# Kernel optimization log

Hardware: AMD Instinct MI355X
Metric: run time of the kernel (lower is better)

The kernel has to match this reference:

```python
import jax, jax.numpy as jnp
import numpy as np

B, S, D = 2, 1024, 1024
N_HEADS = 16
R = 128
M = 8
N_NEURONS = 256


def group_gate(gate, n_basis):
    # gate: [B,S,N] -> [B,S,M], sum over consecutive groups, then normalize
    b, s, n = gate.shape
    gs = n // n_basis  # exact by construction (256/8)
    g = gate.reshape(b, s, n_basis, gs).sum(axis=-1)
    return g / (g.sum(axis=-1, keepdims=True) + 1e-8)


def feature_fn(x, neurons, weights):
    # x:[B,S,D], neurons:[M,D,R], weights:[B,S,M] -> h:[B,S,R]
    all_h = jnp.einsum('bsd,mdr->bsmr', x, neurons)
    return jnp.einsum('bsmr,bsm->bsr', all_h, weights)


def restore_fn(h, neurons, weights):
    # h:[B,S,R], neurons:[M,R,D], weights:[B,S,M] -> [B,S,D]
    pre = jnp.einsum('bsr,bsm->bsmr', h, weights)
    return jnp.einsum('bsmr,mrd->bsd', pre, neurons)


def setup_inputs() -> dict:
    key = jax.random.key(0)
    ks = jax.random.split(key, 9)
    sc = 0.02
    return {
        'x': jax.random.normal(ks[0], (B, S, D), jnp.float32),
        'qk_f': jax.random.normal(ks[1], (M, D, R), jnp.float32) * sc,
        'qk_r': jax.random.normal(ks[2], (M, R, D), jnp.float32) * sc,
        'v_f': jax.random.normal(ks[3], (M, D, R), jnp.float32) * sc,
        'v_r': jax.random.normal(ks[4], (M, R, D), jnp.float32) * sc,
        'Wg_q': jax.random.normal(ks[5], (D, N_NEURONS), jnp.float32) * sc,
        'Wg_k': jax.random.normal(ks[6], (D, N_NEURONS), jnp.float32) * sc,
        'Wg_v': jax.random.normal(ks[7], (D, N_NEURONS), jnp.float32) * sc,
        'W_O': jax.random.normal(ks[8], (D, D), jnp.float32) * sc,
    }


def reference(x, qk_f, qk_r, v_f, v_r, Wg_q, Wg_k, Wg_v, W_O):
    # Router gates (softmax over neuron dim), then grouped per basis
    g_Q = jax.nn.softmax(jnp.einsum('bsd,dn->bsn', x, Wg_q), axis=-1)
    g_K = jax.nn.softmax(jnp.einsum('bsd,dn->bsn', x, Wg_k), axis=-1)
    g_V = jax.nn.softmax(jnp.einsum('bsd,dn->bsn', x, Wg_v), axis=-1)
    gQ_b = group_gate(g_Q, M)
    gK_b = group_gate(g_K, M)
    gV_b = group_gate(g_V, M)

    Q = restore_fn(feature_fn(x, qk_f, gQ_b), qk_r, gQ_b)
    K = restore_fn(feature_fn(x, qk_f, gK_b), qk_r, gK_b)
    V = restore_fn(feature_fn(x, v_f, gV_b), v_r, gV_b)

    d_head = D // N_HEADS
    Q = Q.reshape(B, S, N_HEADS, d_head).transpose(0, 2, 1, 3)
    K = K.reshape(B, S, N_HEADS, d_head).transpose(0, 2, 1, 3)
    V = V.reshape(B, S, N_HEADS, d_head).transpose(0, 2, 1, 3)

    scale = jnp.sqrt(jnp.float32(d_head))
    scores = jnp.einsum('bhsd,bhtd->bhst', Q, K) / scale
    causal = jnp.tril(jnp.ones((S, S), dtype=jnp.bool_))
    scores = jnp.where(causal, scores, jnp.finfo(scores.dtype).min)
    attn_w = jax.nn.softmax(scores, axis=-1)
    out = jnp.einsum('bhst,bhtd->bhsd', attn_w, V)
    out = out.transpose(0, 2, 1, 3).reshape(B, S, D)
    out = jnp.einsum('bsd,de->bse', out, W_O)
    return out
```

## Files before the change

kernel.cpp:

```cpp
#include <hip/hip_runtime.h>
#include <hip/hip_bf16.h>

#define BB 2
#define SS 1024
#define DD 1024
#define NH 16
#define DH 64
#define MM 8
#define RR 128
#define NN 256
#define NT (BB*SS)

using bf16 = __hip_bfloat16;

typedef __attribute__((ext_vector_type(8))) short short8;
typedef __attribute__((ext_vector_type(4))) short short4v;
typedef __attribute__((ext_vector_type(4))) float f32x4;

__device__ __forceinline__ void stf(float* p, size_t i, float v) { p[i] = v; }
__device__ __forceinline__ void stf(bf16* p, size_t i, float v) { p[i] = __float2bfloat16(v); }

#define GLD16(g, l) __builtin_amdgcn_global_load_lds( \
    (const __attribute__((address_space(1))) void*)(g), \
    (__attribute__((address_space(3))) void*)(l), 16, 0, 0)

__device__ __forceinline__ short8 lds_load8(const short* p) {
    short4v a = *(const short4v*)p;
    short4v b = *(const short4v*)(p + 4);
    short8 r;
    r[0] = a[0]; r[1] = a[1]; r[2] = a[2]; r[3] = a[3];
    r[4] = b[0]; r[5] = b[1]; r[6] = b[2]; r[7] = b[3];
    return r;
}

template <typename TC>
__device__ __forceinline__ void gemm64_body(
    const bf16* __restrict__ A, const bf16* __restrict__ Bt, TC* __restrict__ C,
    int Kdim, int Nz, int m0, int n0, bf16* As, bf16* Bs) {
    const int tid = threadIdx.x;
    const int wave = tid >> 6, lane = tid & 63;
    const int quad = lane >> 4, l15 = lane & 15;
    const int wr = wave >> 1, wc = wave & 1;

    f32x4 acc[2][4];
#pragma unroll
    for (int i = 0; i < 2; ++i)
#pragma unroll
        for (int j = 0; j < 4; ++j) acc[i][j] = (f32x4)0.f;

    for (int k0 = 0; k0 < Kdim; k0 += 64) {
        __syncthreads();
#pragma unroll
        for (int i = 0; i < 2; ++i) {
            const int L = i * 256 + wave * 64 + lane;
            const int row = L >> 3;
            const int gch = (L & 7) ^ ((row >> 1) & 7);
            GLD16(A + (size_t)(m0 + row) * Kdim + k0 + gch * 8, &As[(i * 256 + wave * 64) * 8]);
        }
#pragma unroll
        for (int i = 0; i < 4; ++i) {
            const int L = i * 256 + wave * 64 + lane;
            const int row = L >> 3;
            const int gch = (L & 7) ^ ((row >> 1) & 7);
            GLD16(Bt + (size_t)(n0 + row) * Kdim + k0 + gch * 8, &Bs[(i * 256 + wave * 64) * 8]);
        }
        __syncthreads();

#pragma unroll
        for (int kk = 0; kk < 2; ++kk) {
            short8 aF[2], bF[4];
#pragma unroll
            for (int bi = 0; bi < 2; ++bi) {
                int m = wr * 32 + bi * 16 + l15;
                int slot = (kk * 4 + quad) ^ ((m >> 1) & 7);
                aF[bi] = *(const short8*)&As[(m * 8 + slot) * 8];
            }
#pragma unroll
            for (int bj = 0; bj < 4; ++bj) {
                int n = wc * 64 + bj * 16 + l15;
                int slot = (kk * 4 + quad) ^ ((n >> 1) & 7);
                bF[bj] = *(const short8*)&Bs[(n * 8 + slot) * 8];
            }
#pragma unroll
            for (int bi = 0; bi < 2; ++bi)
#pragma unroll
                for (int bj = 0; bj < 4; ++bj)
                    acc[bi][bj] = __builtin_amdgcn_mfma_f32_16x16x32_bf16(aF[bi], bF[bj], acc[bi][bj], 0, 0, 0);
        }
    }

#pragma unroll
    for (int bi = 0; bi < 2; ++bi)
#pragma unroll
        for (int bj = 0; bj < 4; ++bj)
#pragma unroll
            for (int r = 0; r < 4; ++r) {
                int row = m0 + wr * 32 + bi * 16 + quad * 4 + r;
                int col = n0 + wc * 64 + bj * 16 + l15;
                stf(C, (size_t)row * Nz + col, acc[bi][bj][r]);
            }
}

struct GemmZ {
    const bf16* A[5];
    const bf16* Bt[5];
    void* C[5];
    int N[5];
};

__global__ __launch_bounds__(256) void mfma_proj(GemmZ P, int Kdim) {
    __shared__ bf16 As[64 * 64];
    __shared__ bf16 Bs[128 * 64];
    const int wk = (blockIdx.x & 7) * 88 + (blockIdx.x >> 3);
    int z, xx, yy;
    if (wk < 512) { z = wk >> 8; int r = wk & 255; yy = r >> 3; xx = r & 7; }
    else { int r = wk - 512; z = 2 + r / 64; r = r % 64; yy = r >> 1; xx = r & 1; }
    gemm64_body<bf16>(P.A[z], P.Bt[z], (bf16*)P.C[z], Kdim, P.N[z], yy * 64, xx * 128, As, Bs);
}

__global__ __launch_bounds__(256) void mfma_restore(GemmZ P, int Kdim) {
    __shared__ bf16 As[64 * 64];
    __shared__ bf16 Bs[128 * 64];
    const int wk = (blockIdx.x & 7) * 96 + (blockIdx.x >> 3);
    const int z = wk >> 8;
    const int r = wk & 255;
    gemm64_body<bf16>(P.A[z], P.Bt[z], (bf16*)P.C[z], Kdim, P.N[z],
                      (r >> 3) * 64, (r & 7) * 128, As, Bs);
}

__global__ __launch_bounds__(256) void mfma_gemm_64(
    const bf16* __restrict__ A, const bf16* __restrict__ Bt, float* __restrict__ C,
    int Kdim, int Ndim) {
    __shared__ bf16 As[64 * 64];
    __shared__ bf16 Bs[128 * 64];
    const int wk = (blockIdx.x & 7) * 32 + (blockIdx.x >> 3);
    gemm64_body<float>(A, Bt, C, Kdim, Ndim, (wk >> 3) * 64, (wk & 7) * 128, As, Bs);
}

struct ConvJobs {
    const float* src[9];
    bf16* dst[9];
    int K[9], R[9], G[9];
    int tEnd[9];
};

__global__ void convert_kernel(ConvJobs J) {
    __shared__ float tile[32][33];
    const int b = blockIdx.x;
    int j = 0;
    while (j < 8 && b >= J.tEnd[j]) ++j;
    const int local = b - (j > 0 ? J.tEnd[j - 1] : 0);
    const float* src = J.src[j];
    bf16* dst = J.dst[j];
    const int tid = threadIdx.x;

    if (J.G[j] == 0) {
        size_t base = (size_t)local * 4096 + (size_t)tid * 16;
        const float4* s4 = (const float4*)(src + base);
        short* d = (short*)(dst + base);
#pragma unroll
        for (int c = 0; c < 4; ++c) {
            float4 v = s4[c];
            short4v o;
            bf16 t0 = __float2bfloat16(v.x); o[0] = *(short*)&t0;
            bf16 t1 = __float2bfloat16(v.y); o[1] = *(short*)&t1;
            bf16 t2 = __float2bfloat16(v.z); o[2] = *(short*)&t2;
            bf16 t3 = __float2bfloat16(v.w); o[3] = *(short*)&t3;
            *(short4v*)(d + c * 4) = o;
        }
    } else {
        const int Kj = J.K[j], Rj = J.R[j];
        const int Rb = Rj >> 5, Kb = Kj >> 5;
        const int perG = Kb * Rb;
        const int g = local / perG;
        const int rem = local - g * perG;
        const int kb = rem / Rb, rb = rem - kb * Rb;
        const int tx = tid & 31, ty0 = tid >> 5;
        const float* s = src + ((size_t)(g * Kj + kb * 32) * Rj) + rb * 32 + tx;
#pragma unroll
        for (int p = 0; p < 4; ++p)
            tile[ty0 + p * 8][tx] = s[(size_t)(ty0 + p * 8) * Rj];
        __syncthreads();
        bf16* dd = dst + ((size_t)(g * Rj + rb * 32) * Kj) + kb * 32 + tx;
#pragma unroll
        for (int p = 0; p < 4; ++p)
            dd[(size_t)(ty0 + p * 8) * Kj] = __float2bfloat16(tile[tx][ty0 + p * 8]);
    }
}

__global__ void gate_combine(const bf16* __restrict__ logitsAll,
                             const bf16* __restrict__ allh,
                             bf16* __restrict__ preQ, bf16* __restrict__ preK,
                             bf16* __restrict__ preV) {
    const int t = blockIdx.x;
    const int n = threadIdx.x;
    const int wave = n >> 6, lane = n & 63;
    __shared__ float wred[3][4];
    __shared__ float sred[3][4];
    __shared__ float gred[3][8];

    float v[3], e[3];
#pragma unroll
    for (int z = 0; z < 3; ++z)
        v[z] = __bfloat162float(logitsAll[(size_t)z * NT * NN + (size_t)t * NN + n]);

    float mz[3];
#pragma unroll
    for (int z = 0; z < 3; ++z) {
        mz[z] = v[z];
#pragma unroll
        for (int off = 1; off <= 32; off <<= 1)
            mz[z] = fmaxf(mz[z], __shfl_xor(mz[z], off));
    }
    if (lane == 0) {
#pragma unroll
        for (int z = 0; z < 3; ++z) wred[z][wave] = mz[z];
    }
    __syncthreads();
    float gmax[3];
#pragma unroll
    for (int z = 0; z < 3; ++z)
        gmax[z] = fmaxf(fmaxf(wred[z][0], wred[z][1]), fmaxf(wred[z][2], wred[z][3]));

    float ws[3];
#pragma unroll
    for (int z = 0; z < 3; ++z) {
        e[z] = __expf(v[z] - gmax[z]);
        ws[z] = e[z];
#pragma unroll
        for (int off = 1; off <= 32; off <<= 1)
            ws[z] += __shfl_xor(ws[z], off);
    }
    if (lane == 0) {
#pragma unroll
        for (int z = 0; z < 3; ++z) sred[z][wave] = ws[z];
    }
    float gs[3];
#pragma unroll
    for (int z = 0; z < 3; ++z) {
        gs[z] = e[z];
#pragma unroll
        for (int off = 1; off <= 16; off <<= 1)
            gs[z] += __shfl_xor(gs[z], off);
    }
    __syncthreads();
    float total[3];
#pragma unroll
    for (int z = 0; z < 3; ++z)
        total[z] = sred[z][0] + sred[z][1] + sred[z][2] + sred[z][3];
    if ((n & 31) == 0) {
#pragma unroll
        for (int z = 0; z < 3; ++z) gred[z][n >> 5] = gs[z] / total[z];
    }
    __syncthreads();

    float gv[3][8];
#pragma unroll
    for (int z = 0; z < 3; ++z) {
        float tot = 0.f;
#pragma unroll
        for (int m = 0; m < 8; ++m) tot += gred[z][m];
        float inv = 1.0f / (tot + 1e-8f);
#pragma unroll
        for (int m = 0; m < 8; ++m) gv[z][m] = gred[z][m] * inv;
    }

    const int r0 = n & 127;
    const int half = n >> 7;
    const bf16* src_qk = allh + (size_t)t * 1024;
    const bf16* src_v  = allh + (size_t)NT * DD + (size_t)t * 1024;
    float hq = 0.f, hk = 0.f, hv = 0.f;
#pragma unroll
    for (int m = 0; m < 8; ++m) {
        float aqk = __bfloat162float(src_qk[m * 128 + r0]);
        float av  = __bfloat162float(src_v[m * 128 + r0]);
        hq += aqk * gv[0][m];
        hk += aqk * gv[1][m];
        hv += av  * gv[2][m];
    }
    __syncthreads();
#pragma unroll
    for (int mm = 0; mm < 4; ++mm) {
        int m = half * 4 + mm;
        size_t o = (size_t)t * 1024 + m * 128 + r0;
        preQ[o] = __float2bfloat16(hq * gv[0][m]);
        preK[o] = __float2bfloat16(hk * gv[1][m]);
        preV[o] = __float2bfloat16(hv * gv[2][m]);
    }
}

#define LDK 68

__global__ __launch_bounds__(256) void flash_attn_causal(
    const bf16* __restrict__ Q, const bf16* __restrict__ K,
    const bf16* __restrict__ V, bf16* __restrict__ out) {
    const int bx = blockIdx.x;
    const int xcd = bx & 7, slot = bx >> 3;
    const int bh = xcd * 4 + (slot & 3);
    const int qtk = slot >> 2;
    const int qt = (qtk < 8) ? (15 - qtk) : (qtk - 8);
    const int b = bh >> 4;
    const int h = bh & 15;
    const int kt_hi = qt + 1;

    const int tid = threadIdx.x;
    const int wave = tid >> 6;
    const int lane = tid & 63;
    const int quad = lane >> 4;
    const int l15 = lane & 15;

    __shared__ short Ks[2][64 * 64];
    __shared__ short Vt[2][64 * LDK];
    __shared__ short Ps[4 * 16 * LDK];

    const int q_row = qt * 64 + wave * 16 + l15;
    const bf16* qptr = Q + (size_t)(b * SS + q_row) * DD + h * DH + quad * 8;
    short8 aq0 = *(const short8*)qptr;
    short8 aq1 = *(const short8*)(qptr + 32);

    const int krp = tid & 31;
    const int dhb = (tid >> 5) * 8;

    float m_r[4], l_r[4];
    f32x4 o[4];
#pragma unroll
    for (int r = 0; r < 4; ++r) { m_r[r] = -3.0e38f; l_r[r] = 0.f; }
#pragma unroll
    for (int cc = 0; cc < 4; ++cc) o[cc] = (f32x4)0.f;

    const float scale = 0.125f;

    {
#pragma unroll
        for (int i = 0; i < 2; ++i) {
            const int L = i * 256 + wave * 64 + lane;
            const int row = L >> 3;
            const int gch = (L & 7) ^ ((row >> 1) & 7);
            GLD16(K + (size_t)(b * SS + row) * DD + h * DH + gch * 8,
                  &Ks[0][(i * 256 + wave * 64) * 8]);
        }
        const bf16* s0 = V + (size_t)(b * SS + 2 * krp) * DD + h * DH + dhb;
        short8 r0 = *(const short8*)s0;
        short8 r1 = *(const short8*)(s0 + DD);
#pragma unroll
        for (int i = 0; i < 8; ++i) {
            unsigned int pk = (unsigned short)r0[i] | ((unsigned int)(unsigned short)r1[i] << 16);
            *(unsigned int*)&Vt[0][(dhb + i) * LDK + 2 * krp] = pk;
        }
        __syncthreads();
    }

    for (int kt = 0; kt < kt_hi; ++kt) {
        const int buf = kt & 1;
        const bool pf = (kt + 1 < kt_hi);
        short8 pr0, pr1;
        if (pf) {
#pragma unroll
            for (int i = 0; i < 2; ++i) {
                const int L = i * 256 + wave * 64 + lane;
                const int row = L >> 3;
                const int gch = (L & 7) ^ ((row >> 1) & 7);
                GLD16(K + (size_t)(b * SS + (kt + 1) * 64 + row) * DD + h * DH + gch * 8,
                      &Ks[buf ^ 1][(i * 256 + wave * 64) * 8]);
            }
            const bf16* s0 = V + (size_t)(b * SS + (kt + 1) * 64 + 2 * krp) * DD + h * DH + dhb;
            pr0 = *(const short8*)s0;
            pr1 = *(const short8*)(s0 + DD);
        }

        const short* KsB = Ks[buf];
        f32x4 s[4];
#pragma unroll
        for (int cc = 0; cc < 4; ++cc) {
            int n = cc * 16 + l15;
            int sl0 = quad ^ ((n >> 1) & 7);
            int sl1 = (quad + 4) ^ ((n >> 1) & 7);
            short8 bk0 = *(const short8*)&KsB[(n * 8 + sl0) * 8];
            short8 bk1 = *(const short8*)&KsB[(n * 8 + sl1) * 8];
            f32x4 acc = (f32x4)0.f;
            acc = __builtin_amdgcn_mfma_f32_16x16x32_bf16(aq0, bk0, acc, 0, 0, 0);
            acc = __builtin_amdgcn_mfma_f32_16x16x32_bf16(aq1, bk1, acc, 0, 0, 0);
            s[cc] = acc;
        }

        const bool diag = (kt == qt);
#pragma unroll
        for (int cc = 0; cc < 4; ++cc) {
#pragma unroll
            for (int r = 0; r < 4; ++r) {
                float v = s[cc][r] * scale;
                if (diag) {
                    int row_rel = wave * 16 + quad * 4 + r;
                    int col_rel = cc * 16 + l15;
                    if (col_rel > row_rel) v = -3.0e38f;
                }
                s[cc][r] = v;
            }
        }

        float mx[4];
#pragma unroll
        for (int r = 0; r < 4; ++r) {
            float m2 = fmaxf(fmaxf(s[0][r], s[1][r]), fmaxf(s[2][r], s[3][r]));
            m2 = fmaxf(m2, __shfl_xor(m2, 1));
            m2 = fmaxf(m2, __shfl_xor(m2, 2));
            m2 = fmaxf(m2, __shfl_xor(m2, 4));
            m2 = fmaxf(m2, __shfl_xor(m2, 8));
            mx[r] = m2;
        }
        bool grew = false;
#pragma unroll
        for (int r = 0; r < 4; ++r) grew = grew || (mx[r] > m_r[r] + 8.f);
        float alpha[4];
        const bool need = __any(grew);
        if (need) {
#pragma unroll
            for (int r = 0; r < 4; ++r) {
                float nm = fmaxf(m_r[r], mx[r]);
                alpha[r] = __expf(m_r[r] - nm);
                m_r[r] = nm;
            }
        }

        float p[4][4];
#pragma unroll
        for (int r = 0; r < 4; ++r) {
            float rs = 0.f;
#pragma unroll
            for (int cc = 0; cc < 4; ++cc) {
                float e = __expf(s[cc][r] - m_r[r]);
                p[cc][r] = e;
                rs += e;
            }
            rs += __shfl_xor(rs, 1);
            rs += __shfl_xor(rs, 2);
            rs += __shfl_xor(rs, 4);
            rs += __shfl_xor(rs, 8);
            if (need) l_r[r] = l_r[r] * alpha[r] + rs;
            else      l_r[r] += rs;
        }
        if (need) {
#pragma unroll
            for (int cc = 0; cc < 4; ++cc)
#pragma unroll
                for (int r = 0; r < 4; ++r) o[cc][r] *= alpha[r];
        }

        short* pw = &Ps[wave * 16 * LDK];
#pragma unroll
        for (int cc = 0; cc < 4; ++cc)
#pragma unroll
            for (int r = 0; r < 4; ++r) {
                bf16 hb = __float2bfloat16(p[cc][r]);
                pw[(quad * 4 + r) * LDK + cc * 16 + l15] = *(short*)&hb;
            }

        short8 ap0 = lds_load8(&pw[l15 * LDK + quad * 8]);
        short8 ap1 = lds_load8(&pw[l15 * LDK + 32 + quad * 8]);

        const short* VtB = Vt[buf];
#pragma unroll
        for (int cc = 0; cc < 4; ++cc) {
            short8 bv0 = lds_load8(&VtB[(cc * 16 + l15) * LDK + quad * 8]);
            short8 bv1 = lds_load8(&VtB[(cc * 16 + l15) * LDK + 32 + quad * 8]);
            o[cc] = __builtin_amdgcn_mfma_f32_16x16x32_bf16(ap0, bv0, o[cc], 0, 0, 0);
            o[cc] = __builtin_amdgcn_mfma_f32_16x16x32_bf16(ap1, bv1, o[cc], 0, 0, 0);
        }

        if (pf) {
#pragma unroll
            for (int i = 0; i < 8; ++i) {
                unsigned int pk = (unsigned short)pr0[i] | ((unsigned int)(unsigned short)pr1[i] << 16);
                *(unsigned int*)&Vt[buf ^ 1][(dhb + i) * LDK + 2 * krp] = pk;
            }
        }
        __syncthreads();
    }

    float inv[4];
#pragma unroll
    for (int r = 0; r < 4; ++r) inv[r] = 1.0f / l_r[r];
#pragma unroll
    for (int cc = 0; cc < 4; ++cc)
#pragma unroll
        for (int r = 0; r < 4; ++r) {
            int row = qt * 64 + wave * 16 + quad * 4 + r;
            out[(size_t)(b * SS + row) * DD + h * DH + cc * 16 + l15] =
                __float2bfloat16(o[cc][r] * inv[r]);
        }
}

extern "C" void kernel_launch(void* const* d_in, const int* in_sizes, int n_in,
                              void* d_out, int out_size, void* d_ws, size_t ws_size,
                              hipStream_t stream) {
    const float* x    = (const float*)d_in[0];
    const float* qk_f = (const float*)d_in[1];
    const float* qk_r = (const float*)d_in[2];
    const float* v_f  = (const float*)d_in[3];
    const float* v_r  = (const float*)d_in[4];
    const float* Wg_q = (const float*)d_in[5];
    const float* Wg_k = (const float*)d_in[6];
    const float* Wg_v = (const float*)d_in[7];
    const float* W_O  = (const float*)d_in[8];

    char* w = (char*)d_ws;
    const size_t MB = 1 << 20;
    bf16* xb     = (bf16*)(w + 0);
    bf16* wg_bt  = (bf16*)(w + 4 * MB);
    bf16* fbt    = (bf16*)(w + (size_t)(5.5 * MB));
    bf16* logits = (bf16*)(w + (size_t)(9.5 * MB));
    bf16* qkr_bt = (bf16*)(w + 16 * MB);
    bf16* vr_bt  = (bf16*)(w + 18 * MB);
    bf16* wo_bt  = (bf16*)(w + 20 * MB);
    bf16* preQ   = (bf16*)(w + 0);
    bf16* preK   = (bf16*)(w + 4 * MB);
    bf16* Kb     = (bf16*)(w + 8 * MB);
    bf16* Vb     = (bf16*)(w + 12 * MB);
    bf16* attnb  = (bf16*)(w + 0);
    bf16* allh   = (bf16*)d_out;
    bf16* preV   = allh + (size_t)NT * DD;
    bf16* Qb     = (bf16*)d_out;
    float* out   = (float*)d_out;

    ConvJobs J;
    J.src[0] = qk_f; J.dst[0] = fbt;              J.K[0] = 1024; J.R[0] = 128;  J.G[0] = 8;
    J.src[1] = v_f;  J.dst[1] = fbt + 1024*1024;  J.K[1] = 1024; J.R[1] = 128;  J.G[1] = 8;
    J.src[2] = qk_r; J.dst[2] = qkr_bt;           J.K[2] = 1024; J.R[2] = 1024; J.G[2] = 1;
    J.src[3] = v_r;  J.dst[3] = vr_bt;            J.K[3] = 1024; J.R[3] = 1024; J.G[3] = 1;
    J.src[4] = W_O;  J.dst[4] = wo_bt;            J.K[4] = 1024; J.R[4] = 1024; J.G[4] = 1;
    J.src[5] = Wg_q; J.dst[5] = wg_bt;            J.K[5] = 1024; J.R[5] = 256;  J.G[5] = 1;
    J.src[6] = Wg_k; J.dst[6] = wg_bt + 256*1024; J.K[6] = 1024; J.R[6] = 256;  J.G[6] = 1;
    J.src[7] = Wg_v; J.dst[7] = wg_bt + 2*256*1024; J.K[7] = 1024; J.R[7] = 256; J.G[7] = 1;
    J.src[8] = x;    J.dst[8] = xb;               J.K[8] = 0;    J.R[8] = 0;    J.G[8] = 0;
    int tiles[9] = {1024, 1024, 1024, 1024, 1024, 256, 256, 256, 512};
    int cum = 0;
    for (int i = 0; i < 9; ++i) { cum += tiles[i]; J.tEnd[i] = cum; }
    convert_kernel<<<cum, 256, 0, stream>>>(J);

    GemmZ Pp;
    Pp.A[0] = Pp.A[1] = Pp.A[2] = Pp.A[3] = Pp.A[4] = xb;
    Pp.Bt[0] = fbt;             Pp.Bt[1] = fbt + 1024*1024;
    Pp.Bt[2] = wg_bt;           Pp.Bt[3] = wg_bt + 256*1024;  Pp.Bt[4] = wg_bt + 2*256*1024;
    Pp.C[0] = allh;             Pp.C[1] = allh + (size_t)NT * DD;
    Pp.C[2] = logits;           Pp.C[3] = logits + (size_t)NT * NN;
    Pp.C[4] = logits + 2 * (size_t)NT * NN;
    Pp.N[0] = 1024; Pp.N[1] = 1024; Pp.N[2] = 256; Pp.N[3] = 256; Pp.N[4] = 256;
    mfma_proj<<<dim3(704), 256, 0, stream>>>(Pp, DD);

    gate_combine<<<NT, 256, 0, stream>>>(logits, allh, preQ, preK, preV);

    GemmZ Pr;
    Pr.A[0] = preQ; Pr.A[1] = preK; Pr.A[2] = preV;
    Pr.Bt[0] = qkr_bt; Pr.Bt[1] = qkr_bt; Pr.Bt[2] = vr_bt;
    Pr.C[0] = Qb; Pr.C[1] = Kb; Pr.C[2] = Vb;
    Pr.N[0] = Pr.N[1] = Pr.N[2] = 1024;
    Pr.A[3] = Pr.A[4] = nullptr; Pr.Bt[3] = Pr.Bt[4] = nullptr;
    Pr.C[3] = Pr.C[4] = nullptr; Pr.N[3] = Pr.N[4] = 0;
    mfma_restore<<<dim3(768), 256, 0, stream>>>(Pr, DD);

    flash_attn_causal<<<dim3(512), 256, 0, stream>>>(Qb, Kb, Vb, attnb);

    mfma_gemm_64<<<dim3(256), 256, 0, stream>>>(attnb, wo_bt, out, DD, DD);
}
```

Baseline: 193.7 us.

## Fuse dual-B/dual-A GEMMs, merge weight conversion into projection, use exp2 softmax

Several changes at once. The projection GEMM now shares the x tile across both feature weights (dual-B), and the gate logits become a single N=768 GEMM. The transposes of qk_r, v_r and W_O move out of the convert kernel into extra blocks of the projection kernel, so that conversion overlaps the GEMM. The restore GEMM shares the qk_r tile between Q and K (dual-A), the W_O GEMM uses 64x64 tiles to launch more blocks, and flash attention uses exp2 with a log2e-folded scale. The goal is less redundant operand loading, fewer serialized phases and better occupancy, at the cost of more LDS per block and more registers from dual accumulators.

```diff
diff --git a/kernel.cpp b/kernel.cpp
--- a/kernel.cpp
+++ b/kernel.cpp
@@ -17,8 +17,7 @@
 typedef __attribute__((ext_vector_type(4))) short short4v;
 typedef __attribute__((ext_vector_type(4))) float f32x4;
 
-__device__ __forceinline__ void stf(float* p, size_t i, float v) { p[i] = v; }
-__device__ __forceinline__ void stf(bf16* p, size_t i, float v) { p[i] = __float2bfloat16(v); }
+#define EXP2F(x) __builtin_amdgcn_exp2f(x)
 
 #define GLD16(g, l) __builtin_amdgcn_global_load_lds( \
     (const __attribute__((address_space(1))) void*)(g), \
@@ -33,108 +32,299 @@
     return r;
 }
 
-template <typename TC>
-__device__ __forceinline__ void gemm64_body(
-    const bf16* __restrict__ A, const bf16* __restrict__ Bt, TC* __restrict__ C,
-    int Kdim, int Nz, int m0, int n0, bf16* As, bf16* Bs) {
+template <int NR>
+__device__ __forceinline__ void stage_tile(const bf16* __restrict__ src, int k0,
+                                           bf16* lds, int wave, int lane) {
+#pragma unroll
+    for (int i = 0; i < NR / 32; ++i) {
+        const int L = i * 256 + wave * 64 + lane;
+        const int row = L >> 3;
+        const int gch = (L & 7) ^ ((row >> 1) & 7);
+        GLD16(src + (size_t)row * DD + k0 + gch * 8, &lds[(i * 256 + wave * 64) * 8]);
+    }
+}
+
+__device__ __forceinline__ short8 fragld(const bf16* lds, int rc, int kk, int quad) {
+    int slot = (kk * 4 + quad) ^ ((rc >> 1) & 7);
+    return *(const short8*)&((const short*)lds)[(rc * 8 + slot) * 8];
+}
+
+__device__ __forceinline__ void gemm64_std(
+    const bf16* __restrict__ A, const bf16* __restrict__ Bt, bf16* __restrict__ C,
+    int Nz, int m0, int n0, bf16* As, bf16* Bs,
+    int wave, int lane, int quad, int l15) {
+    const int wr = wave >> 1, wc = wave & 1;
+    f32x4 acc[2][4];
+#pragma unroll
+    for (int i = 0; i < 2; ++i)
+#pragma unroll
+        for (int j = 0; j < 4; ++j) acc[i][j] = (f32x4)0.f;
+
+    const bf16* Ab = A + (size_t)m0 * DD;
+    const bf16* Bb = Bt + (size_t)n0 * DD;
+    for (int k0 = 0; k0 < DD; k0 += 64) {
+        __syncthreads();
+        stage_tile<64>(Ab, k0, As, wave, lane);
+        stage_tile<128>(Bb, k0, Bs, wave, lane);
+        __syncthreads();
+#pragma unroll
+        for (int kk = 0; kk < 2; ++kk) {
+            short8 aF[2], bF[4];
+#pragma unroll
+            for (int bi = 0; bi < 2; ++bi) aF[bi] = fragld(As, wr * 32 + bi * 16 + l15, kk, quad);
+#pragma unroll
+            for (int bj = 0; bj < 4; ++bj) bF[bj] = fragld(Bs, wc * 64 + bj * 16 + l15, kk, quad);
+#pragma unroll
+            for (int bi = 0; bi < 2; ++bi)
+#pragma unroll
+                for (int bj = 0; bj < 4; ++bj)
+                    acc[bi][bj] = __builtin_amdgcn_mfma_f32_16x16x32_bf16(aF[bi], bF[bj], acc[bi][bj], 0, 0, 0);
+        }
+    }
+#pragma unroll
+    for (int bi = 0; bi < 2; ++bi)
+#pragma unroll
+        for (int bj = 0; bj < 4; ++bj)
+#pragma unroll
+            for (int r = 0; r < 4; ++r) {
+                int row = m0 + wr * 32 + bi * 16 + quad * 4 + r;
+                int col = n0 + wc * 64 + bj * 16 + l15;
+                C[(size_t)row * Nz + col] = __float2bfloat16(acc[bi][bj][r]);
+            }
+}
+
+__device__ __forceinline__ void gemm64_dualB(
+    const bf16* __restrict__ A, const bf16* __restrict__ B0, const bf16* __restrict__ B1,
+    bf16* __restrict__ C0, bf16* __restrict__ C1,
+    int m0, int n0, bf16* As, bf16* Bs0, bf16* Bs1,
+    int wave, int lane, int quad, int l15) {
+    const int wr = wave >> 1, wc = wave & 1;
+    f32x4 acc0[2][4], acc1[2][4];
+#pragma unroll
+    for (int i = 0; i < 2; ++i)
+#pragma unroll
+        for (int j = 0; j < 4; ++j) { acc0[i][j] = (f32x4)0.f; acc1[i][j] = (f32x4)0.f; }
+
+    const bf16* Ab  = A  + (size_t)m0 * DD;
+    const bf16* B0b = B0 + (size_t)n0 * DD;
+    const bf16* B1b = B1 + (size_t)n0 * DD;
+    for (int k0 = 0; k0 < DD; k0 += 64) {
+        __syncthreads();
+        stage_tile<64>(Ab, k0, As, wave, lane);
+        stage_tile<128>(B0b, k0, Bs0, wave, lane);
+        stage_tile<128>(B1b, k0, Bs1, wave, lane);
+        __syncthreads();
+#pragma unroll
+        for (int kk = 0; kk < 2; ++kk) {
+            short8 aF[2], bF[4];
+#pragma unroll
+            for (int bi = 0; bi < 2; ++bi) aF[bi] = fragld(As, wr * 32 + bi * 16 + l15, kk, quad);
+#pragma unroll
+            for (int bj = 0; bj < 4; ++bj) bF[bj] = fragld(Bs0, wc * 64 + bj * 16 + l15, kk, quad);
+#pragma unroll
+            for (int bi = 0; bi < 2; ++bi)
+#pragma unroll
+                for (int bj = 0; bj < 4; ++bj)
+                    acc0[bi][bj] = __builtin_amdgcn_mfma_f32_16x16x32_bf16(aF[bi], bF[bj], acc0[bi][bj], 0, 0, 0);
+#pragma unroll
+            for (int bj = 0; bj < 4; ++bj) bF[bj] = fragld(Bs1, wc * 64 + bj * 16 + l15, kk, quad);
+#pragma unroll
+            for (int bi = 0; bi < 2; ++bi)
+#pragma unroll
+                for (int bj = 0; bj < 4; ++bj)
+                    acc1[bi][bj] = __builtin_amdgcn_mfma_f32_16x16x32_bf16(aF[bi], bF[bj], acc1[bi][bj], 0, 0, 0);
+        }
+    }
+#pragma unroll
+    for (int bi = 0; bi < 2; ++bi)
+#pragma unroll
+        for (int bj = 0; bj < 4; ++bj)
+#pragma unroll
+            for (int r = 0; r < 4; ++r) {
+                int row = m0 + wr * 32 + bi * 16 + quad * 4 + r;
+                int col = n0 + wc * 64 + bj * 16 + l15;
+                C0[(size_t)row * DD + col] = __float2bfloat16(acc0[bi][bj][r]);
+                C1[(size_t)row * DD + col] = __float2bfloat16(acc1[bi][bj][r]);
+            }
+}
+
+__device__ __forceinline__ void gemm64_dualA(
+    const bf16* __restrict__ A0, const bf16* __restrict__ A1, const bf16* __restrict__ Bt,
+    bf16* __restrict__ C0, bf16* __restrict__ C1,
+    int m0, int n0, bf16* As0, bf16* As1, bf16* Bs,
+    int wave, int lane, int quad, int l15) {
+    const int wr = wave >> 1, wc = wave & 1;
+    f32x4 acc0[2][4], acc1[2][4];
+#pragma unroll
+    for (int i = 0; i < 2; ++i)
+#pragma unroll
+        for (int j = 0; j < 4; ++j) { acc0[i][j] = (f32x4)0.f; acc1[i][j] = (f32x4)0.f; }
+
+    const bf16* A0b = A0 + (size_t)m0 * DD;
+    const bf16* A1b = A1 + (size_t)m0 * DD;
+    const bf16* Bb  = Bt + (size_t)n0 * DD;
+    for (int k0 = 0; k0 < DD; k0 += 64) {
+        __syncthreads();
+        stage_tile<64>(A0b, k0, As0, wave, lane);
+        stage_tile<64>(A1b, k0, As1, wave, lane);
+        stage_tile<128>(Bb, k0, Bs, wave, lane);
+        __syncthreads();
+#pragma unroll
+        for (int kk = 0; kk < 2; ++kk) {
+            short8 aF0[2], aF1[2], bF[4];
+#pragma unroll
+            for (int bi = 0; bi < 2; ++bi) {
+                aF0[bi] = fragld(As0, wr * 32 + bi * 16 + l15, kk, quad);
+                aF1[bi] = fragld(As1, wr * 32 + bi * 16 + l15, kk, quad);
+            }
+#pragma unroll
+            for (int bj = 0; bj < 4; ++bj) bF[bj] = fragld(Bs, wc * 64 + bj * 16 + l15, kk, quad);
+#pragma unroll
+            for (int bi = 0; bi < 2; ++bi)
+#pragma unroll
+                for (int bj = 0; bj < 4; ++bj)
+                    acc0[bi][bj] = __builtin_amdgcn_mfma_f32_16x16x32_bf16(aF0[bi], bF[bj], acc0[bi][bj], 0, 0, 0);
+#pragma unroll
+            for (int bi = 0; bi < 2; ++bi)
+#pragma unroll
+                for (int bj = 0; bj < 4; ++bj)
+                    acc1[bi][bj] = __builtin_amdgcn_mfma_f32_16x16x32_bf16(aF1[bi], bF[bj], acc1[bi][bj], 0, 0, 0);
+        }
+    }
+#pragma unroll
+    for (int bi = 0; bi < 2; ++bi)
+#pragma unroll
+        for (int bj = 0; bj < 4; ++bj)
+#pragma unroll
+            for (int r = 0; r < 4; ++r) {
+                int row = m0 + wr * 32 + bi * 16 + quad * 4 + r;
+                int col = n0 + wc * 64 + bj * 16 + l15;
+                C0[(size_t)row * DD + col] = __float2bfloat16(acc0[bi][bj][r]);
+                C1[(size_t)row * DD + col] = __float2bfloat16(acc1[bi][bj][r]);
+            }
+}
+
+struct ProjArgs {
+    const bf16 *xb, *f0, *f1, *wg;
+    bf16 *allh0, *allh1, *lg;
+    const float* csrc[3];
+    bf16* cdst[3];
+};
+
+__global__ __launch_bounds__(256, 3) void mfma_proj(ProjArgs P) {
+    __shared__ __align__(16) char smem[40960];
+    const int bidx = blockIdx.x;
+    const int tid = threadIdx.x;
+
+    if (bidx >= 448) {
+        float (*tile)[33] = (float(*)[33])smem;
+        const int cb = bidx - 448;
+        const int j = cb >> 10;
+        const int t = cb & 1023;
+        const int kb = t >> 5, rb = t & 31;
+        const int tx = tid & 31, ty0 = tid >> 5;
+        const float* s = P.csrc[j] + ((size_t)(kb * 32) * 1024) + rb * 32 + tx;
+#pragma unroll
+        for (int p = 0; p < 4; ++p)
+            tile[ty0 + p * 8][tx] = s[(size_t)(ty0 + p * 8) * 1024];
+        __syncthreads();
+        bf16* dd = P.cdst[j] + ((size_t)(rb * 32) * 1024) + kb * 32 + tx;
+#pragma unroll
+        for (int p = 0; p < 4; ++p)
+            dd[(size_t)(ty0 + p * 8) * 1024] = __float2bfloat16(tile[tx][ty0 + p * 8]);
+        return;
+    }
+
+    bf16* As  = (bf16*)smem;
+    bf16* Bs0 = As + 64 * 64;
+    bf16* Bs1 = Bs0 + 128 * 64;
+    const int wave = tid >> 6, lane = tid & 63;
+    const int quad = lane >> 4, l15 = lane & 15;
+    const int wk = (bidx & 7) * 56 + (bidx >> 3);
+    if (wk < 256) {
+        const int m0 = (wk >> 3) * 64, n0 = (wk & 7) * 128;
+        gemm64_dualB(P.xb, P.f0, P.f1, P.allh0, P.allh1, m0, n0,
+                     As, Bs0, Bs1, wave, lane, quad, l15);
+    } else {
+        const int r = wk - 256;
+        const int m0 = (r / 6) * 64, n0 = (r % 6) * 128;
+        gemm64_std(P.xb, P.wg, P.lg, 768, m0, n0, As, Bs0, wave, lane, quad, l15);
+    }
+}
+
+struct RestArgs {
+    const bf16 *preQ, *preK, *preV, *qkr, *vr;
+    bf16 *Qb, *Kb, *Vb;
+};
+
+__global__ __launch_bounds__(256, 3) void mfma_restore(RestArgs R) {
+    __shared__ __align__(16) char smem[32768];
+    bf16* As0 = (bf16*)smem;
+    bf16* As1 = As0 + 64 * 64;
+    bf16* Bs  = As1 + 64 * 64;
+    const int tid = threadIdx.x;
+    const int wave = tid >> 6, lane = tid & 63;
+    const int quad = lane >> 4, l15 = lane & 15;
+    const int wk = (blockIdx.x & 7) * 64 + (blockIdx.x >> 3);
+    if (wk < 256) {
+        const int m0 = (wk >> 3) * 64, n0 = (wk & 7) * 128;
+        gemm64_dualA(R.preQ, R.preK, R.qkr, R.Qb, R.Kb, m0, n0,
+                     As0, As1, Bs, wave, lane, quad, l15);
+    } else {
+        const int r = wk - 256;
+        const int m0 = (r >> 3) * 64, n0 = (r & 7) * 128;
+        gemm64_std(R.preV, R.vr, R.Vb, DD, m0, n0, As0, Bs, wave, lane, quad, l15);
+    }
+}
+
+__global__ __launch_bounds__(256) void mfma_wo(
+    const bf16* __restrict__ A, const bf16* __restrict__ Bt, float* __restrict__ C) {
+    __shared__ __align__(16) bf16 As[64 * 64];
+    __shared__ __align__(16) bf16 Bs[64 * 64];
     const int tid = threadIdx.x;
     const int wave = tid >> 6, lane = tid & 63;
     const int quad = lane >> 4, l15 = lane & 15;
     const int wr = wave >> 1, wc = wave & 1;
-
-    f32x4 acc[2][4];
+    const int wk = (blockIdx.x & 7) * 64 + (blockIdx.x >> 3);
+    const int m0 = (wk >> 4) * 64, n0 = (wk & 15) * 64;
+
+    f32x4 acc[2][2];
 #pragma unroll
     for (int i = 0; i < 2; ++i)
 #pragma unroll
-        for (int j = 0; j < 4; ++j) acc[i][j] = (f32x4)0.f;
-
-    for (int k0 = 0; k0 < Kdim; k0 += 64) {
-        __syncthreads();
-#pragma unroll
-        for (int i = 0; i < 2; ++i) {
-            const int L = i * 256 + wave * 64 + lane;
-            const int row = L >> 3;
-            const int gch = (L & 7) ^ ((row >> 1) & 7);
-            GLD16(A + (size_t)(m0 + row) * Kdim + k0 + gch * 8, &As[(i * 256 + wave * 64) * 8]);
-        }
-#pragma unroll
-        for (int i = 0; i < 4; ++i) {
-            const int L = i * 256 + wave * 64 + lane;
-            const int row = L >> 3;
-            const int gch = (L & 7) ^ ((row >> 1) & 7);
-            GLD16(Bt + (size_t)(n0 + row) * Kdim + k0 + gch * 8, &Bs[(i * 256 + wave * 64) * 8]);
-        }
-        __syncthreads();
-
+        for (int j = 0; j < 2; ++j) acc[i][j] = (f32x4)0.f;
+
+    const bf16* Ab = A + (size_t)m0 * DD;
+    const bf16* Bb = Bt + (size_t)n0 * DD;
+    for (int k0 = 0; k0 < DD; k0 += 64) {
+        __syncthreads();
+        stage_tile<64>(Ab, k0, As, wave, lane);
+        stage_tile<64>(Bb, k0, Bs, wave, lane);
+        __syncthreads();
 #pragma unroll
         for (int kk = 0; kk < 2; ++kk) {
-            short8 aF[2], bF[4];
-#pragma unroll
-            for (int bi = 0; bi < 2; ++bi) {
-                int m = wr * 32 + bi * 16 + l15;
-                int slot = (kk * 4 + quad) ^ ((m >> 1) & 7);
-                aF[bi] = *(const short8*)&As[(m * 8 + slot) * 8];
-            }
-#pragma unroll
-            for (int bj = 0; bj < 4; ++bj) {
-                int n = wc * 64 + bj * 16 + l15;
-                int slot = (kk * 4 + quad) ^ ((n >> 1) & 7);
-                bF[bj] = *(const short8*)&Bs[(n * 8 + slot) * 8];
-            }
+            short8 aF[2], bF[2];
+#pragma unroll
+            for (int bi = 0; bi < 2; ++bi) aF[bi] = fragld(As, wr * 32 + bi * 16 + l15, kk, quad);
+#pragma unroll
+            for (int bj = 0; bj < 2; ++bj) bF[bj] = fragld(Bs, wc * 32 + bj * 16 + l15, kk, quad);
 #pragma unroll
             for (int bi = 0; bi < 2; ++bi)
 #pragma unroll
-                for (int bj = 0; bj < 4; ++bj)
+                for (int bj = 0; bj < 2; ++bj)
                     acc[bi][bj] = __builtin_amdgcn_mfma_f32_16x16x32_bf16(aF[bi], bF[bj], acc[bi][bj], 0, 0, 0);
         }
     }
-
 #pragma unroll
     for (int bi = 0; bi < 2; ++bi)
 #pragma unroll
-        for (int bj = 0; bj < 4; ++bj)
+        for (int bj = 0; bj < 2; ++bj)
 #pragma unroll
             for (int r = 0; r < 4; ++r) {
                 int row = m0 + wr * 32 + bi * 16 + quad * 4 + r;
-                int col = n0 + wc * 64 + bj * 16 + l15;
-                stf(C, (size_t)row * Nz + col, acc[bi][bj][r]);
-            }
-}
-
-struct GemmZ {
-    const bf16* A[5];
-    const bf16* Bt[5];
-    void* C[5];
-    int N[5];
-};
-
-__global__ __launch_bounds__(256) void mfma_proj(GemmZ P, int Kdim) {
-    __shared__ bf16 As[64 * 64];
-    __shared__ bf16 Bs[128 * 64];
-    const int wk = (blockIdx.x & 7) * 88 + (blockIdx.x >> 3);
-    int z, xx, yy;
-    if (wk < 512) { z = wk >> 8; int r = wk & 255; yy = r >> 3; xx = r & 7; }
-    else { int r = wk - 512; z = 2 + r / 64; r = r % 64; yy = r >> 1; xx = r & 1; }
-    gemm64_body<bf16>(P.A[z], P.Bt[z], (bf16*)P.C[z], Kdim, P.N[z], yy * 64, xx * 128, As, Bs);
-}
-
-__global__ __launch_bounds__(256) void mfma_restore(GemmZ P, int Kdim) {
-    __shared__ bf16 As[64 * 64];
-    __shared__ bf16 Bs[128 * 64];
-    const int wk = (blockIdx.x & 7) * 96 + (blockIdx.x >> 3);
-    const int z = wk >> 8;
-    const int r = wk & 255;
-    gemm64_body<bf16>(P.A[z], P.Bt[z], (bf16*)P.C[z], Kdim, P.N[z],
-                      (r >> 3) * 64, (r & 7) * 128, As, Bs);
-}
-
-__global__ __launch_bounds__(256) void mfma_gemm_64(
-    const bf16* __restrict__ A, const bf16* __restrict__ Bt, float* __restrict__ C,
-    int Kdim, int Ndim) {
-    __shared__ bf16 As[64 * 64];
-    __shared__ bf16 Bs[128 * 64];
-    const int wk = (blockIdx.x & 7) * 32 + (blockIdx.x >> 3);
-    gemm64_body<float>(A, Bt, C, Kdim, Ndim, (wk >> 3) * 64, (wk & 7) * 128, As, Bs);
+                int col = n0 + wc * 32 + bj * 16 + l15;
+                C[(size_t)row * DD + col] = acc[bi][bj][r];
+            }
 }
 
 struct ConvJobs {
@@ -202,7 +392,7 @@
     float v[3], e[3];
 #pragma unroll
     for (int z = 0; z < 3; ++z)
-        v[z] = __bfloat162float(logitsAll[(size_t)z * NT * NN + (size_t)t * NN + n]);
+        v[z] = __bfloat162float(logitsAll[(size_t)t * 768 + z * 256 + n]);
 
     float mz[3];
 #pragma unroll
@@ -328,7 +518,7 @@
 #pragma unroll
     for (int cc = 0; cc < 4; ++cc) o[cc] = (f32x4)0.f;
 
-    const float scale = 0.125f;
+    const float SCL2 = 0.18033688f;
 
     {
 #pragma unroll
@@ -388,7 +578,7 @@
         for (int cc = 0; cc < 4; ++cc) {
 #pragma unroll
             for (int r = 0; r < 4; ++r) {
-                float v = s[cc][r] * scale;
+                float v = s[cc][r] * SCL2;
                 if (diag) {
                     int row_rel = wave * 16 + quad * 4 + r;
                     int col_rel = cc * 16 + l15;
@@ -417,7 +607,7 @@
 #pragma unroll
             for (int r = 0; r < 4; ++r) {
                 float nm = fmaxf(m_r[r], mx[r]);
-                alpha[r] = __expf(m_r[r] - nm);
+                alpha[r] = EXP2F(m_r[r] - nm);
                 m_r[r] = nm;
             }
         }
@@ -428,7 +618,7 @@
             float rs = 0.f;
 #pragma unroll
             for (int cc = 0; cc < 4; ++cc) {
-                float e = __expf(s[cc][r] - m_r[r]);
+                float e = EXP2F(s[cc][r] - m_r[r]);
                 p[cc][r] = e;
                 rs += e;
             }
@@ -523,42 +713,34 @@
     float* out   = (float*)d_out;
 
     ConvJobs J;
-    J.src[0] = qk_f; J.dst[0] = fbt;              J.K[0] = 1024; J.R[0] = 128;  J.G[0] = 8;
-    J.src[1] = v_f;  J.dst[1] = fbt + 1024*1024;  J.K[1] = 1024; J.R[1] = 128;  J.G[1] = 8;
-    J.src[2] = qk_r; J.dst[2] = qkr_bt;           J.K[2] = 1024; J.R[2] = 1024; J.G[2] = 1;
-    J.src[3] = v_r;  J.dst[3] = vr_bt;            J.K[3] = 1024; J.R[3] = 1024; J.G[3] = 1;
-    J.src[4] = W_O;  J.dst[4] = wo_bt;            J.K[4] = 1024; J.R[4] = 1024; J.G[4] = 1;
-    J.src[5] = Wg_q; J.dst[5] = wg_bt;            J.K[5] = 1024; J.R[5] = 256;  J.G[5] = 1;
-    J.src[6] = Wg_k; J.dst[6] = wg_bt + 256*1024; J.K[6] = 1024; J.R[6] = 256;  J.G[6] = 1;
-    J.src[7] = Wg_v; J.dst[7] = wg_bt + 2*256*1024; J.K[7] = 1024; J.R[7] = 256; J.G[7] = 1;
-    J.src[8] = x;    J.dst[8] = xb;               J.K[8] = 0;    J.R[8] = 0;    J.G[8] = 0;
-    int tiles[9] = {1024, 1024, 1024, 1024, 1024, 256, 256, 256, 512};
+    J.src[0] = x;    J.dst[0] = xb;               J.K[0] = 0;    J.R[0] = 0;    J.G[0] = 0;
+    J.src[1] = qk_f; J.dst[1] = fbt;              J.K[1] = 1024; J.R[1] = 128;  J.G[1] = 8;
+    J.src[2] = v_f;  J.dst[2] = fbt + 1024*1024;  J.K[2] = 1024; J.R[2] = 128;  J.G[2] = 8;
+    J.src[3] = Wg_q; J.dst[3] = wg_bt;            J.K[3] = 1024; J.R[3] = 256;  J.G[3] = 1;
+    J.src[4] = Wg_k; J.dst[4] = wg_bt + 256*1024; J.K[4] = 1024; J.R[4] = 256;  J.G[4] = 1;
+    J.src[5] = Wg_v; J.dst[5] = wg_bt + 2*256*1024; J.K[5] = 1024; J.R[5] = 256; J.G[5] = 1;
+    int tiles[6] = {512, 1024, 1024, 256, 256, 256};
     int cum = 0;
-    for (int i = 0; i < 9; ++i) { cum += tiles[i]; J.tEnd[i] = cum; }
+    for (int i = 0; i < 6; ++i) { cum += tiles[i]; J.tEnd[i] = cum; }
+    for (int i = 6; i < 9; ++i) { J.tEnd[i] = cum; J.src[i] = nullptr; J.dst[i] = nullptr; J.K[i] = J.R[i] = J.G[i] = 0; }
     convert_kernel<<<cum, 256, 0, stream>>>(J);
 
-    GemmZ Pp;
-    Pp.A[0] = Pp.A[1] = Pp.A[2] = Pp.A[3] = Pp.A[4] = xb;
-    Pp.Bt[0] = fbt;             Pp.Bt[1] = fbt + 1024*1024;
-    Pp.Bt[2] = wg_bt;           Pp.Bt[3] = wg_bt + 256*1024;  Pp.Bt[4] = wg_bt + 2*256*1024;
-    Pp.C[0] = allh;             Pp.C[1] = allh + (size_t)NT * DD;
-    Pp.C[2] = logits;           Pp.C[3] = logits + (size_t)NT * NN;
-    Pp.C[4] = logits + 2 * (size_t)NT * NN;
-    Pp.N[0] = 1024; Pp.N[1] = 1024; Pp.N[2] = 256; Pp.N[3] = 256; Pp.N[4] = 256;
-    mfma_proj<<<dim3(704), 256, 0, stream>>>(Pp, DD);
+    ProjArgs Pp;
+    Pp.xb = xb; Pp.f0 = fbt; Pp.f1 = fbt + 1024*1024; Pp.wg = wg_bt;
+    Pp.allh0 = allh; Pp.allh1 = allh + (size_t)NT * DD; Pp.lg = logits;
+    Pp.csrc[0] = qk_r; Pp.csrc[1] = v_r; Pp.csrc[2] = W_O;
+    Pp.cdst[0] = qkr_bt; Pp.cdst[1] = vr_bt; Pp.cdst[2] = wo_bt;
+    mfma_proj<<<dim3(3520), 256, 0, stream>>>(Pp);
 
     gate_combine<<<NT, 256, 0, stream>>>(logits, allh, preQ, preK, preV);
 
-    GemmZ Pr;
-    Pr.A[0] = preQ; Pr.A[1] = preK; Pr.A[2] = preV;
-    Pr.Bt[0] = qkr_bt; Pr.Bt[1] = qkr_bt; Pr.Bt[2] = vr_bt;
-    Pr.C[0] = Qb; Pr.C[1] = Kb; Pr.C[2] = Vb;
-    Pr.N[0] = Pr.N[1] = Pr.N[2] = 1024;
-    Pr.A[3] = Pr.A[4] = nullptr; Pr.Bt[3] = Pr.Bt[4] = nullptr;
-    Pr.C[3] = Pr.C[4] = nullptr; Pr.N[3] = Pr.N[4] = 0;
-    mfma_restore<<<dim3(768), 256, 0, stream>>>(Pr, DD);
+    RestArgs Pr;
+    Pr.preQ = preQ; Pr.preK = preK; Pr.preV = preV;
+    Pr.qkr = qkr_bt; Pr.vr = vr_bt;
+    Pr.Qb = Qb; Pr.Kb = Kb; Pr.Vb = Vb;
+    mfma_restore<<<dim3(512), 256, 0, stream>>>(Pr);
 
     flash_attn_causal<<<dim3(512), 256, 0, stream>>>(Qb, Kb, Vb, attnb);
 
-    mfma_gemm_64<<<dim3(256), 256, 0, stream>>>(attnb, wo_bt, out, DD, DD);
-}
+    mfma_wo<<<dim3(512), 256, 0, stream>>>(attnb, wo_bt, out);
+}
```

After: 193.2 us. Within noise of the previous version (-0.3%).
